# Optimization experiments

Measured on AMD Instinct MI355X. Metric: run time of the kernel, lower is better.

The kernel has to match this reference:

```python
import jax, jax.numpy as jnp
import numpy as np

N, C, K = 65536, 128, 16

def setup_inputs() -> dict:
    key = jax.random.key(0)
    ks = jax.random.split(key, 16)
    def w(k, i, o):
        return jax.random.normal(k, (i, o), dtype=jnp.float32) / np.sqrt(i)
    inp = {
        "x": jax.random.normal(ks[0], (N, C), dtype=jnp.float32),
        "coords": jax.random.normal(ks[1], (N, 3), dtype=jnp.float32) * 10.0,
        "neighbor_idx": jax.random.randint(ks[2], (N, K), 0, N, dtype=jnp.int32),
        # linear_top / linear_down (1x1 Minkowski convs, BN folded into affine)
        "W_top": w(ks[3], C, C), "b_top": jnp.zeros((C,), jnp.float32),
        "W_down": w(ks[4], C, C), "b_down": jnp.zeros((C,), jnp.float32),
        # phi (query), psi (key), alpha (value) 1x1 convs
        "W_phi": w(ks[5], C, C), "b_phi": jnp.zeros((C,), jnp.float32),
        "W_psi": w(ks[6], C, C), "b_psi": jnp.zeros((C,), jnp.float32),
        "W_alpha": w(ks[7], C, C), "b_alpha": jnp.zeros((C,), jnp.float32),
        # delta: positional-encoding MLP on relative xyz (3 -> C -> C)
        "W_d1": w(ks[8], 3, C), "b_d1": jnp.zeros((C,), jnp.float32),
        "W_d2": w(ks[9], C, C), "b_d2": jnp.zeros((C,), jnp.float32),
        # gamma: attention MLP (C -> C -> C), vector attention
        "W_g1": w(ks[10], C, C), "b_g1": jnp.zeros((C,), jnp.float32),
        "W_g2": w(ks[11], C, C), "b_g2": jnp.zeros((C,), jnp.float32),
    }
    return inp

def reference(x, coords, W_top, b_top, W_down, b_down, W_phi, b_phi, W_psi, b_psi,
              W_alpha, b_alpha, W_d1, b_d1, W_d2, b_d2, W_g1, b_g1, W_g2, b_g2,
              neighbor_idx):
    # linear_top
    h = x @ W_top + b_top                                  # (N, C)
    phi = h @ W_phi + b_phi                                # (N, C) query
    psi = h @ W_psi + b_psi                                # (N, C) key
    alpha = h @ W_alpha + b_alpha                          # (N, C) value
    # gather neighbor features / coords (irregular access)
    nb_psi = psi[neighbor_idx]                             # (N, K, C)
    nb_alpha = alpha[neighbor_idx]                         # (N, K, C)
    rel = coords[:, None, :] - coords[neighbor_idx]        # (N, K, 3)
    # delta: relative positional encoding MLP
    pos = jax.nn.relu(rel @ W_d1 + b_d1) @ W_d2 + b_d2     # (N, K, C)
    # vector attention: gamma(phi_i - psi_j + delta)
    attn_in = phi[:, None, :] - nb_psi + pos               # (N, K, C)
    logits = jax.nn.relu(attn_in @ W_g1 + b_g1) @ W_g2 + b_g2
    w = jax.nn.softmax(logits, axis=1)                     # softmax over K neighbors
    y = jnp.sum(w * (nb_alpha + pos), axis=1)              # (N, C)
    # linear_down + residual
    return y @ W_down + b_down + x
```

## Files before the change

kernel.cpp:

```cpp
#include <hip/hip_runtime.h>
#include <math.h>

#define C 128
#define K 16
#define M 4
#define ROWS 64

typedef unsigned short ushort_t;
typedef unsigned int u32;
typedef float f32x4 __attribute__((ext_vector_type(4)));
typedef _Float16 f16x8 __attribute__((ext_vector_type(8)));

union U8h { _Float16 h[8]; uint4 u; };

__device__ __forceinline__ float f16tof(ushort_t b) {
    _Float16 h = __builtin_bit_cast(_Float16, b); return (float)h;
}
__device__ __forceinline__ ushort_t ftof16(float f) {
    _Float16 h = (_Float16)f; return __builtin_bit_cast(ushort_t, h);
}
__device__ __forceinline__ f32x4 mfma16(f16x8 a, f16x8 b, f32x4 c) {
    return __builtin_amdgcn_mfma_f32_16x16x32_f16(a, b, c, 0, 0, 0);
}

__global__ __launch_bounds__(128) void k_prep(
    const float* __restrict__ s0, const float* __restrict__ s1,
    const float* __restrict__ s2, const float* __restrict__ s3,
    ushort_t* __restrict__ d0, ushort_t* __restrict__ d1,
    ushort_t* __restrict__ d2, ushort_t* __restrict__ d3)
{
    const int m = blockIdx.x >> 7, n = blockIdx.x & 127, e = threadIdx.x;
    const float* s = (m==0) ? s0 : (m==1) ? s1 : (m==2) ? s2 : s3;
    ushort_t*   d = (m==0) ? d0 : (m==1) ? d1 : (m==2) ? d2 : d3;
    d[n*C + e] = ftof16(s[e*C + n]);
}

__global__ __launch_bounds__(512) void k_qkv2(
    const float* __restrict__ x,
    const ushort_t* __restrict__ WTt, const float* __restrict__ bt,
    const ushort_t* __restrict__ WTp, const float* __restrict__ bp,
    const ushort_t* __restrict__ WTs, const float* __restrict__ bs,
    const ushort_t* __restrict__ WTa, const float* __restrict__ ba,
    ushort_t* __restrict__ phiB, ushort_t* __restrict__ psiB,
    ushort_t* __restrict__ alfB)
{
    __shared__ ushort_t sX[64*C];
    __shared__ ushort_t sH[64*C];
    const int tid = threadIdx.x, lane = tid & 63, wv = tid >> 6;
    const int ncol = (wv<<4) + (lane&15), arow = lane&15;
    const int kgrp = lane>>4, krow0 = kgrp<<3;
    const int r0 = blockIdx.x * 64;

    {
        const int rX = tid>>3, cX = (tid&7)<<4;
        const float* xp = &x[(size_t)(r0+rX)*C + cX];
        #pragma unroll
        for (int hf = 0; hf < 2; ++hf) {
            const float4 a  = *(const float4*)&xp[hf*8 + 0];
            const float4 b2 = *(const float4*)&xp[hf*8 + 4];
            U8h v;
            v.h[0]=(_Float16)a.x;  v.h[1]=(_Float16)a.y;
            v.h[2]=(_Float16)a.z;  v.h[3]=(_Float16)a.w;
            v.h[4]=(_Float16)b2.x; v.h[5]=(_Float16)b2.y;
            v.h[6]=(_Float16)b2.z; v.h[7]=(_Float16)b2.w;
            const int col = cX + hf*8;
            *(uint4*)&sX[(rX<<7) + (col ^ ((rX&7)<<3))] = v.u;
        }
    }
    __syncthreads();

    {
        f16x8 bf[4]; f32x4 hacc[4];
        #pragma unroll
        for (int kk = 0; kk < 4; ++kk)
            bf[kk] = *(const f16x8*)&WTt[(size_t)ncol*C + (kk<<5) + krow0];
        #pragma unroll
        for (int m = 0; m < 4; ++m) hacc[m] = (f32x4){0.f,0.f,0.f,0.f};
        __builtin_amdgcn_s_setprio(1);
        #pragma unroll
        for (int m = 0; m < 4; ++m)
            #pragma unroll
            for (int kk = 0; kk < 4; ++kk) {
                const int row = (m<<4) + arow;
                const f16x8 af = *(const f16x8*)&sX[(row<<7) + (((kk<<5)+krow0) ^ ((arow&7)<<3))];
                hacc[m] = mfma16(af, bf[kk], hacc[m]);
            }
        __builtin_amdgcn_s_setprio(0);
        const float btc = bt[ncol];
        #pragma unroll
        for (int m = 0; m < 4; ++m)
            #pragma unroll
            for (int r = 0; r < 4; ++r) {
                const int row = (m<<4) + (kgrp<<2) + r;
                sH[(row<<7) + (ncol ^ ((row&7)<<3))] = ftof16(hacc[m][r] + btc);
            }
    }
    __syncthreads();

#define OGEMM(WT_, b_, o_)                                                    \
    {                                                                         \
        f16x8 wf[4]; f32x4 oacc[4];                                           \
        _Pragma("unroll")                                                     \
        for (int kk = 0; kk < 4; ++kk)                                        \
            wf[kk] = *(const f16x8*)&WT_[(size_t)ncol*C + (kk<<5) + krow0];   \
        _Pragma("unroll")                                                     \
        for (int m = 0; m < 4; ++m) oacc[m] = (f32x4){0.f,0.f,0.f,0.f};      \
        __builtin_amdgcn_s_setprio(1);                                        \
        _Pragma("unroll")                                                     \
        for (int m = 0; m < 4; ++m)                                           \
            _Pragma("unroll")                                                 \
            for (int kk = 0; kk < 4; ++kk) {                                  \
                const int row = (m<<4) + arow;                                \
                const f16x8 af = *(const f16x8*)&sH[(row<<7) + (((kk<<5)+krow0) ^ ((arow&7)<<3))]; \
                oacc[m] = mfma16(af, wf[kk], oacc[m]);                        \
            }                                                                 \
        __builtin_amdgcn_s_setprio(0);                                        \
        const float bc = b_[ncol];                                            \
        _Pragma("unroll")                                                     \
        for (int m = 0; m < 4; ++m)                                           \
            _Pragma("unroll")                                                 \
            for (int r = 0; r < 4; ++r) {                                     \
                const int row = (m<<4) + (kgrp<<2) + r;                       \
                o_[(size_t)(r0+row)*C + ncol] = ftof16(oacc[m][r] + bc);      \
            }                                                                 \
    }
    OGEMM(WTp, bp, phiB)
    OGEMM(WTs, bs, psiB)
    OGEMM(WTa, ba, alfB)
#undef OGEMM
}

__global__ __launch_bounds__(512, 4) void k_attn6(
    const ushort_t* __restrict__ phiB, const ushort_t* __restrict__ psiB,
    const ushort_t* __restrict__ alfB,
    const float* __restrict__ coords, const int* __restrict__ nidx,
    const float* __restrict__ Wd1, const float* __restrict__ bd1,
    const ushort_t* __restrict__ WTd2, const float* __restrict__ bd2,
    const ushort_t* __restrict__ WTg1, const float* __restrict__ bg1,
    const ushort_t* __restrict__ WTg2,
    ushort_t* __restrict__ yB,
    int ngroups, int gpb)
{
    __shared__ ushort_t sT0[ROWS*C];
    __shared__ ushort_t sT1[ROWS*C];
    __shared__ ushort_t sA[ROWS*C];
    __shared__ float    sWd1[3][C];
    __shared__ float    sbd1v[C];

    const int tid  = threadIdx.x, lane = tid & 63, wv = tid >> 6;
    const int ncol = (wv<<4) + (lane&15);
    const int arow = lane & 15;
    const int kgrp = lane >> 4, krow0 = kgrp << 3;
    const int grow = tid >> 3;
    const int gpt  = grow >> 4;
    const int gk   = grow & 15;
    const int gc   = (tid & 7) << 4;

    const int g0 = blockIdx.x * gpb;
    if (g0 >= ngroups) return;
    const int gend = (g0 + gpb < ngroups) ? (g0 + gpb) : ngroups;

    if (tid < 3*C) ((float*)sWd1)[tid] = Wd1[tid];
    else if (tid < 4*C) sbd1v[tid - 3*C] = bd1[tid - 3*C];

    f16x8 wd2[4], wg1[4];
    #pragma unroll
    for (int kk = 0; kk < 4; ++kk) {
        wd2[kk] = *(const f16x8*)&WTd2[(size_t)ncol*C + (kk<<5) + krow0];
        wg1[kk] = *(const f16x8*)&WTg1[(size_t)ncol*C + (kk<<5) + krow0];
    }
    const float bd2c = bd2[ncol], bg1c = bg1[ncol];

    __syncthreads();

    int jP; float cn0,cn1,cn2,cj0,cj1,cj2;
    {
        const int pt = g0*M + gpt;
        jP  = nidx[(size_t)pt*K + gk];
        cn0 = coords[(size_t)pt*3+0]; cn1 = coords[(size_t)pt*3+1]; cn2 = coords[(size_t)pt*3+2];
        cj0 = coords[(size_t)jP*3+0]; cj1 = coords[(size_t)jP*3+1]; cj2 = coords[(size_t)jP*3+2];
    }

    const int si0 = (grow<<7) + (gc ^ ((grow&7)<<3));
    const int si1 = (grow<<7) + ((gc+8) ^ ((grow&7)<<3));

    for (int g = g0; g < gend; ++g) {
        const int p0 = g * M;
        const bool hn = (g + 1 < gend);

        {
            const float rx = cn0 - cj0, ry = cn1 - cj1, rz = cn2 - cj2;
            #pragma unroll
            for (int hf = 0; hf < 2; ++hf) {
                U8h hi, lo;
                #pragma unroll
                for (int z = 0; z < 8; ++z) {
                    const int c = gc + (hf<<3) + z;
                    float t = fmaf(rx, sWd1[0][c],
                              fmaf(ry, sWd1[1][c],
                              fmaf(rz, sWd1[2][c], sbd1v[c])));
                    t = fmaxf(t, 0.f);
                    hi.h[z] = (_Float16)t;
                    lo.h[z] = (_Float16)(t - (float)hi.h[z]);
                }
                const int si = hf ? si1 : si0;
                *(uint4*)&sT0[si] = hi.u;
                *(uint4*)&sT1[si] = lo.u;
            }
        }
        __syncthreads();

        ushort_t phv[M];
        ushort_t psv[M][4];
        #pragma unroll
        for (int m = 0; m < M; ++m) {
            phv[m] = phiB[(size_t)(p0+m)*C + ncol];
            const int4 j4 = *(const int4*)&nidx[(size_t)(p0+m)*K + (kgrp<<2)];
            psv[m][0] = psiB[(size_t)j4.x*C + ncol];
            psv[m][1] = psiB[(size_t)j4.y*C + ncol];
            psv[m][2] = psiB[(size_t)j4.z*C + ncol];
            psv[m][3] = psiB[(size_t)j4.w*C + ncol];
        }

        f32x4 pos[M];
        #pragma unroll
        for (int m = 0; m < M; ++m) pos[m] = (f32x4){0.f,0.f,0.f,0.f};
        __builtin_amdgcn_s_setprio(1);
        #pragma unroll
        for (int m = 0; m < M; ++m)
            #pragma unroll
            for (int kk = 0; kk < 4; ++kk) {
                const int si = (((m<<4)+arow)<<7) + (((kk<<5)+krow0) ^ ((arow&7)<<3));
                pos[m] = mfma16(*(const f16x8*)&sT0[si], wd2[kk], pos[m]);
                pos[m] = mfma16(*(const f16x8*)&sT1[si], wd2[kk], pos[m]);
            }
        __builtin_amdgcn_s_setprio(0);

        #pragma unroll
        for (int m = 0; m < M; ++m) {
            #pragma unroll
            for (int z = 0; z < 4; ++z) pos[m][z] += bd2c;
            const float phic = f16tof(phv[m]);
            #pragma unroll
            for (int r = 0; r < 4; ++r) {
                const int row = (m<<4) + (kgrp<<2) + r;
                const float av = phic - f16tof(psv[m][r]) + pos[m][r];
                sA[(row<<7) + (ncol ^ ((row&7)<<3))] = ftof16(av);
            }
        }
        __syncthreads();

        ushort_t alv[M][4];
        #pragma unroll
        for (int m = 0; m < M; ++m) {
            const int4 j4 = *(const int4*)&nidx[(size_t)(p0+m)*K + (kgrp<<2)];
            alv[m][0] = alfB[(size_t)j4.x*C + ncol];
            alv[m][1] = alfB[(size_t)j4.y*C + ncol];
            alv[m][2] = alfB[(size_t)j4.z*C + ncol];
            alv[m][3] = alfB[(size_t)j4.w*C + ncol];
        }
        f16x8 wg2s[4];
        #pragma unroll
        for (int kk = 0; kk < 4; ++kk)
            wg2s[kk] = *(const f16x8*)&WTg2[(size_t)ncol*C + (kk<<5) + krow0];

        {
            f32x4 ua[M];
            #pragma unroll
            for (int m = 0; m < M; ++m) ua[m] = (f32x4){0.f,0.f,0.f,0.f};
            __builtin_amdgcn_s_setprio(1);
            #pragma unroll
            for (int m = 0; m < M; ++m)
                #pragma unroll
                for (int kk = 0; kk < 4; ++kk) {
                    const int si = (((m<<4)+arow)<<7) + (((kk<<5)+krow0) ^ ((arow&7)<<3));
                    ua[m] = mfma16(*(const f16x8*)&sA[si], wg1[kk], ua[m]);
                }
            __builtin_amdgcn_s_setprio(0);
            #pragma unroll
            for (int m = 0; m < M; ++m)
                #pragma unroll
                for (int r = 0; r < 4; ++r) {
                    const int row = (m<<4) + (kgrp<<2) + r;
                    sT1[(row<<7) + (ncol ^ ((row&7)<<3))] =
                        ftof16(fmaxf(ua[m][r] + bg1c, 0.f));
                }
        }
        if (hn) {
            const int pt = (g+1)*M + gpt;
            jP  = nidx[(size_t)pt*K + gk];
            cn0 = coords[(size_t)pt*3+0]; cn1 = coords[(size_t)pt*3+1]; cn2 = coords[(size_t)pt*3+2];
            cj0 = coords[(size_t)jP*3+0]; cj1 = coords[(size_t)jP*3+1]; cj2 = coords[(size_t)jP*3+2];
        }
        __syncthreads();

        f32x4 lg[M];
        #pragma unroll
        for (int m = 0; m < M; ++m) lg[m] = (f32x4){0.f,0.f,0.f,0.f};
        __builtin_amdgcn_s_setprio(1);
        #pragma unroll
        for (int m = 0; m < M; ++m)
            #pragma unroll
            for (int kk = 0; kk < 4; ++kk) {
                const int si = (((m<<4)+arow)<<7) + (((kk<<5)+krow0) ^ ((arow&7)<<3));
                lg[m] = mfma16(*(const f16x8*)&sT1[si], wg2s[kk], lg[m]);
            }
        __builtin_amdgcn_s_setprio(0);

        #pragma unroll
        for (int m = 0; m < M; ++m) {
            float mx = fmaxf(fmaxf(lg[m][0], lg[m][1]), fmaxf(lg[m][2], lg[m][3]));
            mx = fmaxf(mx, __shfl_xor(mx, 16));
            mx = fmaxf(mx, __shfl_xor(mx, 32));
            const float e0 = __expf(lg[m][0]-mx), e1 = __expf(lg[m][1]-mx);
            const float e2 = __expf(lg[m][2]-mx), e3 = __expf(lg[m][3]-mx);
            float den = e0 + e1 + e2 + e3;
            den += __shfl_xor(den, 16);
            den += __shfl_xor(den, 32);
            const float inv = 1.0f / den;
            float yp;
            yp  = e0 * (f16tof(alv[m][0]) + pos[m][0]);
            yp += e1 * (f16tof(alv[m][1]) + pos[m][1]);
            yp += e2 * (f16tof(alv[m][2]) + pos[m][2]);
            yp += e3 * (f16tof(alv[m][3]) + pos[m][3]);
            yp *= inv;
            yp += __shfl_xor(yp, 16);
            yp += __shfl_xor(yp, 32);
            if (lane < 16)
                yB[(size_t)(p0+m)*C + ncol] = ftof16(yp);
        }
        __syncthreads();
    }
}

__global__ __launch_bounds__(512) void k_down(
    const ushort_t* __restrict__ yB,
    const ushort_t* __restrict__ WTdn, const float* __restrict__ bdn,
    const float* __restrict__ x, float* __restrict__ out)
{
    __shared__ ushort_t sY[64*C];
    const int tid = threadIdx.x, lane = tid & 63, wv = tid >> 6;
    const int ncol = (wv<<4) + (lane&15), arow = lane&15;
    const int kgrp = lane>>4, krow0 = kgrp<<3;
    const int r0 = blockIdx.x * 64;

    {
        const int rY = tid>>3, cY = (tid&7)<<4;
        #pragma unroll
        for (int hf = 0; hf < 2; ++hf) {
            const uint4 v = *(const uint4*)&yB[(size_t)(r0+rY)*C + cY + hf*8];
            *(uint4*)&sY[(rY<<7) + ((cY + hf*8) ^ ((rY&7)<<3))] = v;
        }
    }
    __syncthreads();

    f16x8 wf[4]; f32x4 oacc[4];
    #pragma unroll
    for (int kk = 0; kk < 4; ++kk)
        wf[kk] = *(const f16x8*)&WTdn[(size_t)ncol*C + (kk<<5) + krow0];
    #pragma unroll
    for (int m = 0; m < 4; ++m) oacc[m] = (f32x4){0.f,0.f,0.f,0.f};
    __builtin_amdgcn_s_setprio(1);
    #pragma unroll
    for (int m = 0; m < 4; ++m)
        #pragma unroll
        for (int kk = 0; kk < 4; ++kk) {
            const int row = (m<<4) + arow;
            const f16x8 af = *(const f16x8*)&sY[(row<<7) + (((kk<<5)+krow0) ^ ((arow&7)<<3))];
            oacc[m] = mfma16(af, wf[kk], oacc[m]);
        }
    __builtin_amdgcn_s_setprio(0);
    const float bc = bdn[ncol];
    #pragma unroll
    for (int m = 0; m < 4; ++m)
        #pragma unroll
        for (int r = 0; r < 4; ++r) {
            const int row = (m<<4) + (kgrp<<2) + r;
            const size_t idx = (size_t)(r0+row)*C + ncol;
            out[idx] = oacc[m][r] + bc + x[idx];
        }
}

extern "C" void kernel_launch(void* const* d_in, const int* in_sizes, int n_in,
                              void* d_out, int out_size, void* d_ws, size_t ws_size,
                              hipStream_t stream)
{
    const float* x      = (const float*)d_in[0];
    const float* coords = (const float*)d_in[1];
    const int*   nidx   = (const int*)d_in[2];
    const float* W_top  = (const float*)d_in[3];
    const float* b_top  = (const float*)d_in[4];
    const float* W_down = (const float*)d_in[5];
    const float* b_down = (const float*)d_in[6];
    const float* W_phi  = (const float*)d_in[7];
    const float* b_phi  = (const float*)d_in[8];
    const float* W_psi  = (const float*)d_in[9];
    const float* b_psi  = (const float*)d_in[10];
    const float* W_alpha= (const float*)d_in[11];
    const float* b_alpha= (const float*)d_in[12];
    const float* W_d1   = (const float*)d_in[13];
    const float* b_d1   = (const float*)d_in[14];
    const float* W_d2   = (const float*)d_in[15];
    const float* b_d2   = (const float*)d_in[16];
    const float* W_g1   = (const float*)d_in[17];
    const float* b_g1   = (const float*)d_in[18];
    const float* W_g2   = (const float*)d_in[19];
    const float* b_g2   = (const float*)d_in[20];
    (void)b_g2;

    const int N = in_sizes[0] / C;

    ushort_t* WTt  = (ushort_t*)d_ws;
    ushort_t* WTp  = WTt  + C*C;
    ushort_t* WTs  = WTp  + C*C;
    ushort_t* WTa  = WTs  + C*C;
    ushort_t* WTd2 = WTa  + C*C;
    ushort_t* WTg1 = WTd2 + C*C;
    ushort_t* WTg2 = WTg1 + C*C;
    ushort_t* WTdn = WTg2 + C*C;
    ushort_t* phiB = WTdn + C*C;
    ushort_t* psiB = phiB + (size_t)N*C;
    ushort_t* alfB = psiB + (size_t)N*C;
    ushort_t* yB   = alfB + (size_t)N*C;
    float* out = (float*)d_out;

    hipLaunchKernelGGL(k_prep, dim3(4*C), dim3(C), 0, stream,
        W_top, W_phi, W_psi, W_alpha, WTt, WTp, WTs, WTa);
    hipLaunchKernelGGL(k_prep, dim3(4*C), dim3(C), 0, stream,
        W_d2, W_g1, W_g2, W_down, WTd2, WTg1, WTg2, WTdn);

    hipLaunchKernelGGL(k_qkv2, dim3(N / 64), dim3(512), 0, stream,
        x, WTt, b_top, WTp, b_phi, WTs, b_psi, WTa, b_alpha,
        phiB, psiB, alfB);

    const int ngroups = N / M;
    const int NBLK = 2048;
    const int gpb = (ngroups + NBLK - 1) / NBLK;
    hipLaunchKernelGGL(k_attn6, dim3(NBLK), dim3(512), 0, stream,
        phiB, psiB, alfB, coords, nidx,
        W_d1, b_d1, WTd2, b_d2, WTg1, b_g1, WTg2,
        yB, ngroups, gpb);

    hipLaunchKernelGGL(k_down, dim3(N / 64), dim3(512), 0, stream,
        yB, WTdn, b_down, x, out);
}
```

Measured before the change: 542.2 us.

## Halve attention block to 256 threads with two column tiles per wave

The attention kernel now runs 4 waves per block instead of 8. Each wave covers two 16-column output tiles (col0 and col0+64), so every A-fragment read from LDS feeds two MFMAs. The Wd2/Wg1 weight fragments are now reloaded from global memory on each group iteration instead of being held in registers across the loop, which trades register pressure for extra (likely cached) loads. Per-thread work in the relu/split stage doubles, and occupancy changes through the new launch bounds and the unchanged LDS footprint per block.

```diff
diff --git a/kernel.cpp b/kernel.cpp
--- a/kernel.cpp
+++ b/kernel.cpp
@@ -130,7 +130,7 @@
 #undef OGEMM
 }
 
-__global__ __launch_bounds__(512, 4) void k_attn6(
+__global__ __launch_bounds__(256, 3) void k_attn8(
     const ushort_t* __restrict__ phiB, const ushort_t* __restrict__ psiB,
     const ushort_t* __restrict__ alfB,
     const float* __restrict__ coords, const int* __restrict__ nidx,
@@ -144,32 +144,26 @@
     __shared__ ushort_t sT0[ROWS*C];
     __shared__ ushort_t sT1[ROWS*C];
     __shared__ ushort_t sA[ROWS*C];
-    __shared__ float    sWd1[3][C];
-    __shared__ float    sbd1v[C];
+    __shared__ float    sW1b[512];
 
     const int tid  = threadIdx.x, lane = tid & 63, wv = tid >> 6;
-    const int ncol = (wv<<4) + (lane&15);
+    const int col0 = (wv<<4) + (lane&15);
     const int arow = lane & 15;
     const int kgrp = lane >> 4, krow0 = kgrp << 3;
-    const int grow = tid >> 3;
+    const int grow = tid >> 2;
     const int gpt  = grow >> 4;
     const int gk   = grow & 15;
-    const int gc   = (tid & 7) << 4;
+    const int gc   = (tid & 3) << 5;
 
     const int g0 = blockIdx.x * gpb;
     if (g0 >= ngroups) return;
     const int gend = (g0 + gpb < ngroups) ? (g0 + gpb) : ngroups;
 
-    if (tid < 3*C) ((float*)sWd1)[tid] = Wd1[tid];
-    else if (tid < 4*C) sbd1v[tid - 3*C] = bd1[tid - 3*C];
-
-    f16x8 wd2[4], wg1[4];
-    #pragma unroll
-    for (int kk = 0; kk < 4; ++kk) {
-        wd2[kk] = *(const f16x8*)&WTd2[(size_t)ncol*C + (kk<<5) + krow0];
-        wg1[kk] = *(const f16x8*)&WTg1[(size_t)ncol*C + (kk<<5) + krow0];
-    }
-    const float bd2c = bd2[ncol], bg1c = bg1[ncol];
+    for (int i = tid; i < 512; i += 256)
+        sW1b[i] = (i < 384) ? Wd1[i] : bd1[i - 384];
+
+    const float bd2c0 = bd2[col0],    bd2c1 = bd2[col0+64];
+    const float bg1c0 = bg1[col0],    bg1c1 = bg1[col0+64];
 
     __syncthreads();
 
@@ -181,9 +175,6 @@
         cj0 = coords[(size_t)jP*3+0]; cj1 = coords[(size_t)jP*3+1]; cj2 = coords[(size_t)jP*3+2];
     }
 
-    const int si0 = (grow<<7) + (gc ^ ((grow&7)<<3));
-    const int si1 = (grow<<7) + ((gc+8) ^ ((grow&7)<<3));
-
     for (int g = g0; g < gend; ++g) {
         const int p0 = g * M;
         const bool hn = (g + 1 < gend);
@@ -191,90 +182,107 @@
         {
             const float rx = cn0 - cj0, ry = cn1 - cj1, rz = cn2 - cj2;
             #pragma unroll
-            for (int hf = 0; hf < 2; ++hf) {
+            for (int s = 0; s < 4; ++s) {
                 U8h hi, lo;
                 #pragma unroll
                 for (int z = 0; z < 8; ++z) {
-                    const int c = gc + (hf<<3) + z;
-                    float t = fmaf(rx, sWd1[0][c],
-                              fmaf(ry, sWd1[1][c],
-                              fmaf(rz, sWd1[2][c], sbd1v[c])));
+                    const int c = gc + (s<<3) + z;
+                    float t = fmaf(rx, sW1b[c],
+                              fmaf(ry, sW1b[128+c],
+                              fmaf(rz, sW1b[256+c], sW1b[384+c])));
                     t = fmaxf(t, 0.f);
                     hi.h[z] = (_Float16)t;
                     lo.h[z] = (_Float16)(t - (float)hi.h[z]);
                 }
-                const int si = hf ? si1 : si0;
+                const int si = (grow<<7) + ((gc + (s<<3)) ^ ((grow&7)<<3));
                 *(uint4*)&sT0[si] = hi.u;
                 *(uint4*)&sT1[si] = lo.u;
             }
         }
         __syncthreads();
 
-        ushort_t phv[M];
-        ushort_t psv[M][4];
+        ushort_t phv[M][2];
+        ushort_t psv[M][4][2];
         #pragma unroll
         for (int m = 0; m < M; ++m) {
-            phv[m] = phiB[(size_t)(p0+m)*C + ncol];
+            phv[m][0] = phiB[(size_t)(p0+m)*C + col0];
+            phv[m][1] = phiB[(size_t)(p0+m)*C + col0 + 64];
             const int4 j4 = *(const int4*)&nidx[(size_t)(p0+m)*K + (kgrp<<2)];
-            psv[m][0] = psiB[(size_t)j4.x*C + ncol];
-            psv[m][1] = psiB[(size_t)j4.y*C + ncol];
-            psv[m][2] = psiB[(size_t)j4.z*C + ncol];
-            psv[m][3] = psiB[(size_t)j4.w*C + ncol];
-        }
-
-        f32x4 pos[M];
-        #pragma unroll
-        for (int m = 0; m < M; ++m) pos[m] = (f32x4){0.f,0.f,0.f,0.f};
+            psv[m][0][0] = psiB[(size_t)j4.x*C + col0];
+            psv[m][0][1] = psiB[(size_t)j4.x*C + col0 + 64];
+            psv[m][1][0] = psiB[(size_t)j4.y*C + col0];
+            psv[m][1][1] = psiB[(size_t)j4.y*C + col0 + 64];
+            psv[m][2][0] = psiB[(size_t)j4.z*C + col0];
+            psv[m][2][1] = psiB[(size_t)j4.z*C + col0 + 64];
+            psv[m][3][0] = psiB[(size_t)j4.w*C + col0];
+            psv[m][3][1] = psiB[(size_t)j4.w*C + col0 + 64];
+        }
+
+        f16x8 w0[4], w1[4];
+        #pragma unroll
+        for (int kk = 0; kk < 4; ++kk) {
+            w0[kk] = *(const f16x8*)&WTd2[(size_t)col0*C      + (kk<<5) + krow0];
+            w1[kk] = *(const f16x8*)&WTd2[(size_t)(col0+64)*C + (kk<<5) + krow0];
+        }
+
+        f32x4 pos[M][2];
+        #pragma unroll
+        for (int m = 0; m < M; ++m) {
+            pos[m][0] = (f32x4){0.f,0.f,0.f,0.f};
+            pos[m][1] = (f32x4){0.f,0.f,0.f,0.f};
+        }
         __builtin_amdgcn_s_setprio(1);
         #pragma unroll
         for (int m = 0; m < M; ++m)
             #pragma unroll
             for (int kk = 0; kk < 4; ++kk) {
                 const int si = (((m<<4)+arow)<<7) + (((kk<<5)+krow0) ^ ((arow&7)<<3));
-                pos[m] = mfma16(*(const f16x8*)&sT0[si], wd2[kk], pos[m]);
-                pos[m] = mfma16(*(const f16x8*)&sT1[si], wd2[kk], pos[m]);
+                const f16x8 ah = *(const f16x8*)&sT0[si];
+                const f16x8 al = *(const f16x8*)&sT1[si];
+                pos[m][0] = mfma16(ah, w0[kk], pos[m][0]);
+                pos[m][1] = mfma16(ah, w1[kk], pos[m][1]);
+                pos[m][0] = mfma16(al, w0[kk], pos[m][0]);
+                pos[m][1] = mfma16(al, w1[kk], pos[m][1]);
             }
         __builtin_amdgcn_s_setprio(0);
 
         #pragma unroll
         for (int m = 0; m < M; ++m) {
             #pragma unroll
-            for (int z = 0; z < 4; ++z) pos[m][z] += bd2c;
-            const float phic = f16tof(phv[m]);
+            for (int z = 0; z < 4; ++z) { pos[m][0][z] += bd2c0; pos[m][1][z] += bd2c1; }
+            const float ph0 = f16tof(phv[m][0]), ph1 = f16tof(phv[m][1]);
             #pragma unroll
             for (int r = 0; r < 4; ++r) {
                 const int row = (m<<4) + (kgrp<<2) + r;
-                const float av = phic - f16tof(psv[m][r]) + pos[m][r];
-                sA[(row<<7) + (ncol ^ ((row&7)<<3))] = ftof16(av);
+                const int sw  = (row&7)<<3;
+                sA[(row<<7) + ( col0       ^ sw)] = ftof16(ph0 - f16tof(psv[m][r][0]) + pos[m][0][r]);
+                sA[(row<<7) + ((col0 + 64) ^ sw)] = ftof16(ph1 - f16tof(psv[m][r][1]) + pos[m][1][r]);
             }
         }
         __syncthreads();
 
-        ushort_t alv[M][4];
-        #pragma unroll
-        for (int m = 0; m < M; ++m) {
-            const int4 j4 = *(const int4*)&nidx[(size_t)(p0+m)*K + (kgrp<<2)];
-            alv[m][0] = alfB[(size_t)j4.x*C + ncol];
-            alv[m][1] = alfB[(size_t)j4.y*C + ncol];
-            alv[m][2] = alfB[(size_t)j4.z*C + ncol];
-            alv[m][3] = alfB[(size_t)j4.w*C + ncol];
-        }
-        f16x8 wg2s[4];
-        #pragma unroll
-        for (int kk = 0; kk < 4; ++kk)
-            wg2s[kk] = *(const f16x8*)&WTg2[(size_t)ncol*C + (kk<<5) + krow0];
-
         {
-            f32x4 ua[M];
-            #pragma unroll
-            for (int m = 0; m < M; ++m) ua[m] = (f32x4){0.f,0.f,0.f,0.f};
+            f16x8 g10[4], g11[4];
+            #pragma unroll
+            for (int kk = 0; kk < 4; ++kk) {
+                g10[kk] = *(const f16x8*)&WTg1[(size_t)col0*C      + (kk<<5) + krow0];
+                g11[kk] = *(const f16x8*)&WTg1[(size_t)(col0+64)*C + (kk<<5) + krow0];
+            }
+            f32x4 ua[M][2];
+            #pragma unroll
+            for (int m = 0; m < M; ++m) {
+                ua[m][0] = (f32x4){0.f,0.f,0.f,0.f};
+                ua[m][1] = (f32x4){0.f,0.f,0.f,0.f};
+            }
             __builtin_amdgcn_s_setprio(1);
             #pragma unroll
             for (int m = 0; m < M; ++m)
                 #pragma unroll
                 for (int kk = 0; kk < 4; ++kk) {
                     const int si = (((m<<4)+arow)<<7) + (((kk<<5)+krow0) ^ ((arow&7)<<3));
-                    ua[m] = mfma16(*(const f16x8*)&sA[si], wg1[kk], ua[m]);
+                    const f16x8 a = *(const f16x8*)&sA[si];
+                    ua[m][0] = mfma16(a, g10[kk], ua[m][0]);
+                    ua[m][1] = mfma16(a, g11[kk], ua[m][1]);
                 }
             __builtin_amdgcn_s_setprio(0);
             #pragma unroll
@@ -282,8 +290,9 @@
                 #pragma unroll
                 for (int r = 0; r < 4; ++r) {
                     const int row = (m<<4) + (kgrp<<2) + r;
-                    sT1[(row<<7) + (ncol ^ ((row&7)<<3))] =
-                        ftof16(fmaxf(ua[m][r] + bg1c, 0.f));
+                    const int sw  = (row&7)<<3;
+                    sT1[(row<<7) + ( col0       ^ sw)] = ftof16(fmaxf(ua[m][0][r] + bg1c0, 0.f));
+                    sT1[(row<<7) + ((col0 + 64) ^ sw)] = ftof16(fmaxf(ua[m][1][r] + bg1c1, 0.f));
                 }
         }
         if (hn) {
@@ -294,41 +303,69 @@
         }
         __syncthreads();
 
-        f32x4 lg[M];
-        #pragma unroll
-        for (int m = 0; m < M; ++m) lg[m] = (f32x4){0.f,0.f,0.f,0.f};
+        ushort_t alv[M][4][2];
+        #pragma unroll
+        for (int m = 0; m < M; ++m) {
+            const int4 j4 = *(const int4*)&nidx[(size_t)(p0+m)*K + (kgrp<<2)];
+            alv[m][0][0] = alfB[(size_t)j4.x*C + col0];
+            alv[m][0][1] = alfB[(size_t)j4.x*C + col0 + 64];
+            alv[m][1][0] = alfB[(size_t)j4.y*C + col0];
+            alv[m][1][1] = alfB[(size_t)j4.y*C + col0 + 64];
+            alv[m][2][0] = alfB[(size_t)j4.z*C + col0];
+            alv[m][2][1] = alfB[(size_t)j4.z*C + col0 + 64];
+            alv[m][3][0] = alfB[(size_t)j4.w*C + col0];
+            alv[m][3][1] = alfB[(size_t)j4.w*C + col0 + 64];
+        }
+        f16x8 g20[4], g21[4];
+        #pragma unroll
+        for (int kk = 0; kk < 4; ++kk) {
+            g20[kk] = *(const f16x8*)&WTg2[(size_t)col0*C      + (kk<<5) + krow0];
+            g21[kk] = *(const f16x8*)&WTg2[(size_t)(col0+64)*C + (kk<<5) + krow0];
+        }
+
+        f32x4 lg[M][2];
+        #pragma unroll
+        for (int m = 0; m < M; ++m) {
+            lg[m][0] = (f32x4){0.f,0.f,0.f,0.f};
+            lg[m][1] = (f32x4){0.f,0.f,0.f,0.f};
+        }
         __builtin_amdgcn_s_setprio(1);
         #pragma unroll
         for (int m = 0; m < M; ++m)
             #pragma unroll
             for (int kk = 0; kk < 4; ++kk) {
                 const int si = (((m<<4)+arow)<<7) + (((kk<<5)+krow0) ^ ((arow&7)<<3));
-                lg[m] = mfma16(*(const f16x8*)&sT1[si], wg2s[kk], lg[m]);
+                const f16x8 a = *(const f16x8*)&sT1[si];
+                lg[m][0] = mfma16(a, g20[kk], lg[m][0]);
+                lg[m][1] = mfma16(a, g21[kk], lg[m][1]);
             }
         __builtin_amdgcn_s_setprio(0);
 
         #pragma unroll
-        for (int m = 0; m < M; ++m) {
-            float mx = fmaxf(fmaxf(lg[m][0], lg[m][1]), fmaxf(lg[m][2], lg[m][3]));
-            mx = fmaxf(mx, __shfl_xor(mx, 16));
-            mx = fmaxf(mx, __shfl_xor(mx, 32));
-            const float e0 = __expf(lg[m][0]-mx), e1 = __expf(lg[m][1]-mx);
-            const float e2 = __expf(lg[m][2]-mx), e3 = __expf(lg[m][3]-mx);
-            float den = e0 + e1 + e2 + e3;
-            den += __shfl_xor(den, 16);
-            den += __shfl_xor(den, 32);
-            const float inv = 1.0f / den;
-            float yp;
-            yp  = e0 * (f16tof(alv[m][0]) + pos[m][0]);
-            yp += e1 * (f16tof(alv[m][1]) + pos[m][1]);
-            yp += e2 * (f16tof(alv[m][2]) + pos[m][2]);
-            yp += e3 * (f16tof(alv[m][3]) + pos[m][3]);
-            yp *= inv;
-            yp += __shfl_xor(yp, 16);
-            yp += __shfl_xor(yp, 32);
-            if (lane < 16)
-                yB[(size_t)(p0+m)*C + ncol] = ftof16(yp);
-        }
+        for (int m = 0; m < M; ++m)
+            #pragma unroll
+            for (int ct = 0; ct < 2; ++ct) {
+                const f32x4 l = lg[m][ct];
+                float mx = fmaxf(fmaxf(l[0], l[1]), fmaxf(l[2], l[3]));
+                mx = fmaxf(mx, __shfl_xor(mx, 16));
+                mx = fmaxf(mx, __shfl_xor(mx, 32));
+                const float e0 = __expf(l[0]-mx), e1 = __expf(l[1]-mx);
+                const float e2 = __expf(l[2]-mx), e3 = __expf(l[3]-mx);
+                float den = e0 + e1 + e2 + e3;
+                den += __shfl_xor(den, 16);
+                den += __shfl_xor(den, 32);
+                const float inv = 1.0f / den;
+                float yp;
+                yp  = e0 * (f16tof(alv[m][0][ct]) + pos[m][ct][0]);
+                yp += e1 * (f16tof(alv[m][1][ct]) + pos[m][ct][1]);
+                yp += e2 * (f16tof(alv[m][2][ct]) + pos[m][ct][2]);
+                yp += e3 * (f16tof(alv[m][3][ct]) + pos[m][ct][3]);
+                yp *= inv;
+                yp += __shfl_xor(yp, 16);
+                yp += __shfl_xor(yp, 32);
+                if (lane < 16)
+                    yB[(size_t)(p0+m)*C + col0 + (ct<<6)] = ftof16(yp);
+            }
         __syncthreads();
     }
 }
@@ -436,7 +473,7 @@
     const int ngroups = N / M;
     const int NBLK = 2048;
     const int gpb = (ngroups + NBLK - 1) / NBLK;
-    hipLaunchKernelGGL(k_attn6, dim3(NBLK), dim3(512), 0, stream,
+    hipLaunchKernelGGL(k_attn8, dim3(NBLK), dim3(256), 0, stream,
         phiB, psiB, alfB, coords, nidx,
         W_d1, b_d1, WTd2, b_d2, WTg1, b_g1, WTg2,
         yB, ngroups, gpb);
```

Result: slower. 893.9 us (+64.9%).

## Restructure attention kernel to one point per wavefront without block barriers

Applied to the files above, without the earlier changes.

Replaces the block-cooperative attention kernel, where 8 waves split output columns over 4-point groups and sync with __syncthreads, with a per-wave design. Each wave processes one point's 16 neighbors across all 128 columns using private LDS tiles, so no block barriers are needed. Weights are now streamed from global or L2 per column tile instead of held in registers. The hi/lo fp16 split of the positional hidden layer is dropped, which lowers precision, and the grid shrinks to 768 blocks of 256 threads with a grid-stride loop. The aim is to remove barrier stalls and register pressure, at the cost of more repeated weight loads and lower MFMA reuse per load.

```diff
diff --git a/kernel.cpp b/kernel.cpp
--- a/kernel.cpp
+++ b/kernel.cpp
@@ -3,8 +3,6 @@
 
 #define C 128
 #define K 16
-#define M 4
-#define ROWS 64
 
 typedef unsigned short ushort_t;
 typedef unsigned int u32;
@@ -130,7 +128,7 @@
 #undef OGEMM
 }
 
-__global__ __launch_bounds__(512, 4) void k_attn6(
+__global__ __launch_bounds__(256, 2) void k_attn_w(
     const ushort_t* __restrict__ phiB, const ushort_t* __restrict__ psiB,
     const ushort_t* __restrict__ alfB,
     const float* __restrict__ coords, const int* __restrict__ nidx,
@@ -138,198 +136,169 @@
     const ushort_t* __restrict__ WTd2, const float* __restrict__ bd2,
     const ushort_t* __restrict__ WTg1, const float* __restrict__ bg1,
     const ushort_t* __restrict__ WTg2,
-    ushort_t* __restrict__ yB,
-    int ngroups, int gpb)
+    ushort_t* __restrict__ yB, int npts)
 {
-    __shared__ ushort_t sT0[ROWS*C];
-    __shared__ ushort_t sT1[ROWS*C];
-    __shared__ ushort_t sA[ROWS*C];
-    __shared__ float    sWd1[3][C];
-    __shared__ float    sbd1v[C];
-
-    const int tid  = threadIdx.x, lane = tid & 63, wv = tid >> 6;
-    const int ncol = (wv<<4) + (lane&15);
-    const int arow = lane & 15;
-    const int kgrp = lane >> 4, krow0 = kgrp << 3;
-    const int grow = tid >> 3;
-    const int gpt  = grow >> 4;
-    const int gk   = grow & 15;
-    const int gc   = (tid & 7) << 4;
-
-    const int g0 = blockIdx.x * gpb;
-    if (g0 >= ngroups) return;
-    const int gend = (g0 + gpb < ngroups) ? (g0 + gpb) : ngroups;
-
-    if (tid < 3*C) ((float*)sWd1)[tid] = Wd1[tid];
-    else if (tid < 4*C) sbd1v[tid - 3*C] = bd1[tid - 3*C];
-
-    f16x8 wd2[4], wg1[4];
-    #pragma unroll
-    for (int kk = 0; kk < 4; ++kk) {
-        wd2[kk] = *(const f16x8*)&WTd2[(size_t)ncol*C + (kk<<5) + krow0];
-        wg1[kk] = *(const f16x8*)&WTg1[(size_t)ncol*C + (kk<<5) + krow0];
-    }
-    const float bd2c = bd2[ncol], bg1c = bg1[ncol];
-
+    __shared__ ushort_t sT[4][16*C];
+    __shared__ ushort_t sA[4][16*C];
+    __shared__ ushort_t sP[4][16*C];
+    __shared__ float    sW1b[512];
+
+    const int tid  = threadIdx.x, lane = tid & 63, wid = tid >> 6;
+    ushort_t* T = sT[wid];
+    ushort_t* A = sA[wid];
+    ushort_t* P = sP[wid];
+
+    for (int i = tid; i < 512; i += 256)
+        sW1b[i] = (i < 384) ? Wd1[i] : bd1[i - 384];
     __syncthreads();
 
-    int jP; float cn0,cn1,cn2,cj0,cj1,cj2;
-    {
-        const int pt = g0*M + gpt;
-        jP  = nidx[(size_t)pt*K + gk];
-        cn0 = coords[(size_t)pt*3+0]; cn1 = coords[(size_t)pt*3+1]; cn2 = coords[(size_t)pt*3+2];
-        cj0 = coords[(size_t)jP*3+0]; cj1 = coords[(size_t)jP*3+1]; cj2 = coords[(size_t)jP*3+2];
-    }
-
-    const int si0 = (grow<<7) + (gc ^ ((grow&7)<<3));
-    const int si1 = (grow<<7) + ((gc+8) ^ ((grow&7)<<3));
-
-    for (int g = g0; g < gend; ++g) {
-        const int p0 = g * M;
-        const bool hn = (g + 1 < gend);
-
+    const int arow  = lane & 15;
+    const int kgrp  = lane >> 4;
+    const int krow0 = kgrp << 3;
+    const int rb    = kgrp << 2;
+    const int trow  = lane >> 2;
+    const int tcol  = (lane & 3) << 5;
+
+    const int gw     = blockIdx.x * 4 + wid;
+    const int stride = gridDim.x * 4;
+
+    for (int p = gw; p < npts; p += stride) {
         {
-            const float rx = cn0 - cj0, ry = cn1 - cj1, rz = cn2 - cj2;
+            const int jt = nidx[(size_t)p*K + trow];
+            const float rx = coords[(size_t)p*3+0] - coords[(size_t)jt*3+0];
+            const float ry = coords[(size_t)p*3+1] - coords[(size_t)jt*3+1];
+            const float rz = coords[(size_t)p*3+2] - coords[(size_t)jt*3+2];
             #pragma unroll
-            for (int hf = 0; hf < 2; ++hf) {
-                U8h hi, lo;
+            for (int s = 0; s < 4; ++s) {
+                U8h h;
                 #pragma unroll
                 for (int z = 0; z < 8; ++z) {
-                    const int c = gc + (hf<<3) + z;
-                    float t = fmaf(rx, sWd1[0][c],
-                              fmaf(ry, sWd1[1][c],
-                              fmaf(rz, sWd1[2][c], sbd1v[c])));
-                    t = fmaxf(t, 0.f);
-                    hi.h[z] = (_Float16)t;
-                    lo.h[z] = (_Float16)(t - (float)hi.h[z]);
+                    const int c = tcol + (s<<3) + z;
+                    float t = fmaf(rx, sW1b[c],
+                              fmaf(ry, sW1b[128+c],
+                              fmaf(rz, sW1b[256+c], sW1b[384+c])));
+                    h.h[z] = (_Float16)fmaxf(t, 0.f);
                 }
-                const int si = hf ? si1 : si0;
-                *(uint4*)&sT0[si] = hi.u;
-                *(uint4*)&sT1[si] = lo.u;
-            }
-        }
-        __syncthreads();
-
-        ushort_t phv[M];
-        ushort_t psv[M][4];
-        #pragma unroll
-        for (int m = 0; m < M; ++m) {
-            phv[m] = phiB[(size_t)(p0+m)*C + ncol];
-            const int4 j4 = *(const int4*)&nidx[(size_t)(p0+m)*K + (kgrp<<2)];
-            psv[m][0] = psiB[(size_t)j4.x*C + ncol];
-            psv[m][1] = psiB[(size_t)j4.y*C + ncol];
-            psv[m][2] = psiB[(size_t)j4.z*C + ncol];
-            psv[m][3] = psiB[(size_t)j4.w*C + ncol];
-        }
-
-        f32x4 pos[M];
-        #pragma unroll
-        for (int m = 0; m < M; ++m) pos[m] = (f32x4){0.f,0.f,0.f,0.f};
-        __builtin_amdgcn_s_setprio(1);
-        #pragma unroll
-        for (int m = 0; m < M; ++m)
-            #pragma unroll
-            for (int kk = 0; kk < 4; ++kk) {
-                const int si = (((m<<4)+arow)<<7) + (((kk<<5)+krow0) ^ ((arow&7)<<3));
-                pos[m] = mfma16(*(const f16x8*)&sT0[si], wd2[kk], pos[m]);
-                pos[m] = mfma16(*(const f16x8*)&sT1[si], wd2[kk], pos[m]);
-            }
-        __builtin_amdgcn_s_setprio(0);
-
-        #pragma unroll
-        for (int m = 0; m < M; ++m) {
-            #pragma unroll
-            for (int z = 0; z < 4; ++z) pos[m][z] += bd2c;
-            const float phic = f16tof(phv[m]);
-            #pragma unroll
-            for (int r = 0; r < 4; ++r) {
-                const int row = (m<<4) + (kgrp<<2) + r;
-                const float av = phic - f16tof(psv[m][r]) + pos[m][r];
-                sA[(row<<7) + (ncol ^ ((row&7)<<3))] = ftof16(av);
-            }
-        }
-        __syncthreads();
-
-        ushort_t alv[M][4];
-        #pragma unroll
-        for (int m = 0; m < M; ++m) {
-            const int4 j4 = *(const int4*)&nidx[(size_t)(p0+m)*K + (kgrp<<2)];
-            alv[m][0] = alfB[(size_t)j4.x*C + ncol];
-            alv[m][1] = alfB[(size_t)j4.y*C + ncol];
-            alv[m][2] = alfB[(size_t)j4.z*C + ncol];
-            alv[m][3] = alfB[(size_t)j4.w*C + ncol];
-        }
-        f16x8 wg2s[4];
-        #pragma unroll
-        for (int kk = 0; kk < 4; ++kk)
-            wg2s[kk] = *(const f16x8*)&WTg2[(size_t)ncol*C + (kk<<5) + krow0];
+                *(uint4*)&T[(trow<<7) + ((tcol + (s<<3)) ^ ((trow&7)<<3))] = h.u;
+            }
+        }
+
+        const int4 j4 = *(const int4*)&nidx[(size_t)p*K + rb];
 
         {
-            f32x4 ua[M];
-            #pragma unroll
-            for (int m = 0; m < M; ++m) ua[m] = (f32x4){0.f,0.f,0.f,0.f};
-            __builtin_amdgcn_s_setprio(1);
-            #pragma unroll
-            for (int m = 0; m < M; ++m)
-                #pragma unroll
-                for (int kk = 0; kk < 4; ++kk) {
-                    const int si = (((m<<4)+arow)<<7) + (((kk<<5)+krow0) ^ ((arow&7)<<3));
-                    ua[m] = mfma16(*(const f16x8*)&sA[si], wg1[kk], ua[m]);
-                }
-            __builtin_amdgcn_s_setprio(0);
-            #pragma unroll
-            for (int m = 0; m < M; ++m)
+            f16x8 af0 = *(const f16x8*)&T[(arow<<7) + (( 0 + krow0) ^ ((arow&7)<<3))];
+            f16x8 af1 = *(const f16x8*)&T[(arow<<7) + ((32 + krow0) ^ ((arow&7)<<3))];
+            f16x8 af2 = *(const f16x8*)&T[(arow<<7) + ((64 + krow0) ^ ((arow&7)<<3))];
+            f16x8 af3 = *(const f16x8*)&T[(arow<<7) + ((96 + krow0) ^ ((arow&7)<<3))];
+            #pragma unroll 2
+            for (int ct = 0; ct < 8; ++ct) {
+                const int col = (ct<<4) + arow;
+                const ushort_t* wp = &WTd2[(size_t)col*C + krow0];
+                const f16x8 w0 = *(const f16x8*)&wp[0];
+                const f16x8 w1 = *(const f16x8*)&wp[32];
+                const f16x8 w2 = *(const f16x8*)&wp[64];
+                const f16x8 w3 = *(const f16x8*)&wp[96];
+                const float bd2c = bd2[col];
+                const ushort_t phv = phiB[(size_t)p*C + col];
+                const ushort_t ps0 = psiB[(size_t)j4.x*C + col];
+                const ushort_t ps1 = psiB[(size_t)j4.y*C + col];
+                const ushort_t ps2 = psiB[(size_t)j4.z*C + col];
+                const ushort_t ps3 = psiB[(size_t)j4.w*C + col];
+                f32x4 acc = (f32x4){0.f,0.f,0.f,0.f};
+                acc = mfma16(af0, w0, acc);
+                acc = mfma16(af1, w1, acc);
+                acc = mfma16(af2, w2, acc);
+                acc = mfma16(af3, w3, acc);
+                const float ph = f16tof(phv);
                 #pragma unroll
                 for (int r = 0; r < 4; ++r) {
-                    const int row = (m<<4) + (kgrp<<2) + r;
-                    sT1[(row<<7) + (ncol ^ ((row&7)<<3))] =
-                        ftof16(fmaxf(ua[m][r] + bg1c, 0.f));
+                    const int row = rb + r;
+                    const int si  = (row<<7) + (col ^ ((row&7)<<3));
+                    const float pv = acc[r] + bd2c;
+                    P[si] = ftof16(pv);
+                    const float psr = (r==0) ? f16tof(ps0) : (r==1) ? f16tof(ps1)
+                                    : (r==2) ? f16tof(ps2) : f16tof(ps3);
+                    A[si] = ftof16(ph - psr + pv);
                 }
-        }
-        if (hn) {
-            const int pt = (g+1)*M + gpt;
-            jP  = nidx[(size_t)pt*K + gk];
-            cn0 = coords[(size_t)pt*3+0]; cn1 = coords[(size_t)pt*3+1]; cn2 = coords[(size_t)pt*3+2];
-            cj0 = coords[(size_t)jP*3+0]; cj1 = coords[(size_t)jP*3+1]; cj2 = coords[(size_t)jP*3+2];
-        }
-        __syncthreads();
-
-        f32x4 lg[M];
-        #pragma unroll
-        for (int m = 0; m < M; ++m) lg[m] = (f32x4){0.f,0.f,0.f,0.f};
-        __builtin_amdgcn_s_setprio(1);
-        #pragma unroll
-        for (int m = 0; m < M; ++m)
-            #pragma unroll
-            for (int kk = 0; kk < 4; ++kk) {
-                const int si = (((m<<4)+arow)<<7) + (((kk<<5)+krow0) ^ ((arow&7)<<3));
-                lg[m] = mfma16(*(const f16x8*)&sT1[si], wg2s[kk], lg[m]);
-            }
-        __builtin_amdgcn_s_setprio(0);
-
-        #pragma unroll
-        for (int m = 0; m < M; ++m) {
-            float mx = fmaxf(fmaxf(lg[m][0], lg[m][1]), fmaxf(lg[m][2], lg[m][3]));
-            mx = fmaxf(mx, __shfl_xor(mx, 16));
-            mx = fmaxf(mx, __shfl_xor(mx, 32));
-            const float e0 = __expf(lg[m][0]-mx), e1 = __expf(lg[m][1]-mx);
-            const float e2 = __expf(lg[m][2]-mx), e3 = __expf(lg[m][3]-mx);
-            float den = e0 + e1 + e2 + e3;
-            den += __shfl_xor(den, 16);
-            den += __shfl_xor(den, 32);
-            const float inv = 1.0f / den;
-            float yp;
-            yp  = e0 * (f16tof(alv[m][0]) + pos[m][0]);
-            yp += e1 * (f16tof(alv[m][1]) + pos[m][1]);
-            yp += e2 * (f16tof(alv[m][2]) + pos[m][2]);
-            yp += e3 * (f16tof(alv[m][3]) + pos[m][3]);
-            yp *= inv;
-            yp += __shfl_xor(yp, 16);
-            yp += __shfl_xor(yp, 32);
-            if (lane < 16)
-                yB[(size_t)(p0+m)*C + ncol] = ftof16(yp);
-        }
-        __syncthreads();
+            }
+        }
+
+        {
+            f16x8 ag0 = *(const f16x8*)&A[(arow<<7) + (( 0 + krow0) ^ ((arow&7)<<3))];
+            f16x8 ag1 = *(const f16x8*)&A[(arow<<7) + ((32 + krow0) ^ ((arow&7)<<3))];
+            f16x8 ag2 = *(const f16x8*)&A[(arow<<7) + ((64 + krow0) ^ ((arow&7)<<3))];
+            f16x8 ag3 = *(const f16x8*)&A[(arow<<7) + ((96 + krow0) ^ ((arow&7)<<3))];
+            #pragma unroll 2
+            for (int ct = 0; ct < 8; ++ct) {
+                const int col = (ct<<4) + arow;
+                const ushort_t* wp = &WTg1[(size_t)col*C + krow0];
+                const f16x8 w0 = *(const f16x8*)&wp[0];
+                const f16x8 w1 = *(const f16x8*)&wp[32];
+                const f16x8 w2 = *(const f16x8*)&wp[64];
+                const f16x8 w3 = *(const f16x8*)&wp[96];
+                const float bg1c = bg1[col];
+                f32x4 acc = (f32x4){0.f,0.f,0.f,0.f};
+                acc = mfma16(ag0, w0, acc);
+                acc = mfma16(ag1, w1, acc);
+                acc = mfma16(ag2, w2, acc);
+                acc = mfma16(ag3, w3, acc);
+                #pragma unroll
+                for (int r = 0; r < 4; ++r) {
+                    const int row = rb + r;
+                    T[(row<<7) + (col ^ ((row&7)<<3))] =
+                        ftof16(fmaxf(acc[r] + bg1c, 0.f));
+                }
+            }
+        }
+
+        {
+            f16x8 au0 = *(const f16x8*)&T[(arow<<7) + (( 0 + krow0) ^ ((arow&7)<<3))];
+            f16x8 au1 = *(const f16x8*)&T[(arow<<7) + ((32 + krow0) ^ ((arow&7)<<3))];
+            f16x8 au2 = *(const f16x8*)&T[(arow<<7) + ((64 + krow0) ^ ((arow&7)<<3))];
+            f16x8 au3 = *(const f16x8*)&T[(arow<<7) + ((96 + krow0) ^ ((arow&7)<<3))];
+            #pragma unroll 2
+            for (int ct = 0; ct < 8; ++ct) {
+                const int col = (ct<<4) + arow;
+                const ushort_t* wp = &WTg2[(size_t)col*C + krow0];
+                const f16x8 w0 = *(const f16x8*)&wp[0];
+                const f16x8 w1 = *(const f16x8*)&wp[32];
+                const f16x8 w2 = *(const f16x8*)&wp[64];
+                const f16x8 w3 = *(const f16x8*)&wp[96];
+                const ushort_t a0 = alfB[(size_t)j4.x*C + col];
+                const ushort_t a1 = alfB[(size_t)j4.y*C + col];
+                const ushort_t a2 = alfB[(size_t)j4.z*C + col];
+                const ushort_t a3 = alfB[(size_t)j4.w*C + col];
+                f32x4 lg = (f32x4){0.f,0.f,0.f,0.f};
+                lg = mfma16(au0, w0, lg);
+                lg = mfma16(au1, w1, lg);
+                lg = mfma16(au2, w2, lg);
+                lg = mfma16(au3, w3, lg);
+                float mx = fmaxf(fmaxf(lg[0], lg[1]), fmaxf(lg[2], lg[3]));
+                mx = fmaxf(mx, __shfl_xor(mx, 16));
+                mx = fmaxf(mx, __shfl_xor(mx, 32));
+                const float e0 = __expf(lg[0]-mx), e1 = __expf(lg[1]-mx);
+                const float e2 = __expf(lg[2]-mx), e3 = __expf(lg[3]-mx);
+                float den = e0 + e1 + e2 + e3;
+                den += __shfl_xor(den, 16);
+                den += __shfl_xor(den, 32);
+                const float inv = 1.0f / den;
+                float yp = 0.f;
+                #pragma unroll
+                for (int r = 0; r < 4; ++r) {
+                    const int row = rb + r;
+                    const float pr = f16tof(P[(row<<7) + (col ^ ((row&7)<<3))]);
+                    const float av = (r==0) ? f16tof(a0) : (r==1) ? f16tof(a1)
+                                   : (r==2) ? f16tof(a2) : f16tof(a3);
+                    const float ee = (r==0) ? e0 : (r==1) ? e1 : (r==2) ? e2 : e3;
+                    yp = fmaf(ee, av + pr, yp);
+                }
+                yp *= inv;
+                yp += __shfl_xor(yp, 16);
+                yp += __shfl_xor(yp, 32);
+                if (lane < 16)
+                    yB[(size_t)p*C + col] = ftof16(yp);
+            }
+        }
     }
 }
 
@@ -433,13 +402,10 @@
         x, WTt, b_top, WTp, b_phi, WTs, b_psi, WTa, b_alpha,
         phiB, psiB, alfB);
 
-    const int ngroups = N / M;
-    const int NBLK = 2048;
-    const int gpb = (ngroups + NBLK - 1) / NBLK;
-    hipLaunchKernelGGL(k_attn6, dim3(NBLK), dim3(512), 0, stream,
+    hipLaunchKernelGGL(k_attn_w, dim3(768), dim3(256), 0, stream,
         phiB, psiB, alfB, coords, nidx,
         W_d1, b_d1, WTd2, b_d2, WTg1, b_g1, WTg2,
-        yB, ngroups, gpb);
+        yB, N);
 
     hipLaunchKernelGGL(k_down, dim3(N / 64), dim3(512), 0, stream,
         yB, WTdn, b_down, x, out);
```

After: 920.8 us. 1.7x slower.
